# Optimization experiments

Measured on AMD Instinct MI355X. Metric: run time of the kernel, lower is better.

The kernel has to match this reference:

```python
import jax, jax.numpy as jnp
import numpy as np

TEMPERATURE = 0.07
EPS = 1e-12  # matches torch F.normalize eps default

def setup_inputs() -> dict:
    key = jax.random.key(0)
    k1, k2 = jax.random.split(key)
    emb_i = jax.random.normal(k1, (4096, 256), dtype=jnp.float32)
    emb_j = jax.random.normal(k2, (4096, 256), dtype=jnp.float32)
    return {"emb_i": emb_i, "emb_j": emb_j}

def reference(emb_i, emb_j):
    N = emb_i.shape[0]
    # L2-normalize each embedding (F.normalize, dim=1)
    def l2n(x):
        return x / jnp.maximum(jnp.linalg.norm(x, axis=1, keepdims=True), EPS)
    z = jnp.concatenate([l2n(emb_i), l2n(emb_j)], axis=0)  # [2N, D]
    # cosine similarity of normalized rows == plain dot product
    sim = z @ z.T  # [2N, 2N]
    idx = jnp.arange(N)
    pos = jnp.concatenate([sim[idx, idx + N], sim[idx + N, idx]], axis=0)  # [2N]
    exp_sim = jnp.exp(sim / TEMPERATURE)
    # denominator: all entries in the row except the self (diagonal) term
    denom = jnp.sum(exp_sim, axis=1) - jnp.diagonal(exp_sim)  # [2N]
    loss_pair = -(pos / TEMPERATURE) + jnp.log(denom)
    return jnp.sum(loss_pair) / (2 * N)
```

## Files before the change

kernel.cpp:

```cpp
#include <hip/hip_runtime.h>
#include <hip/hip_bf16.h>

#define N_ROWS 4096
#define TWO_N  8192
#define D      256
#define DB     512

#define K_SQRT_SCALE 4.5398159980773926f
#define K_LN2        0.6931471805599453f

#define WAVES        4
#define ROWS_PER_WAVE 64
#define BLOCK_ROWS   (WAVES * ROWS_PER_WAVE)
#define COL_CHUNK    512
#define STAGE_COLS   64
#define NSTAGES      (COL_CHUNK / STAGE_COLS)

typedef __attribute__((ext_vector_type(8))) short short8;
typedef __attribute__((ext_vector_type(4))) float f32x4;

static __device__ inline unsigned short f2bf(float x) {
    __hip_bfloat16 h = __float2bfloat16(x);
    return __builtin_bit_cast(unsigned short, h);
}

__global__ __launch_bounds__(256) void normalize_kernel(
        const float* __restrict__ emb_i, const float* __restrict__ emb_j,
        unsigned short* __restrict__ z, float* __restrict__ S) {
    const int gtid = blockIdx.x * 256 + threadIdx.x;
    if (gtid < TWO_N) S[gtid] = 0.0f;

    const int row  = gtid >> 6;
    const int lane = threadIdx.x & 63;
    if (row >= TWO_N) return;

    const float* src = (row < N_ROWS) ? emb_i + (size_t)row * D
                                      : emb_j + (size_t)(row - N_ROWS) * D;
    float4 v = reinterpret_cast<const float4*>(src)[lane];
    float ss = v.x * v.x + v.y * v.y + v.z * v.z + v.w * v.w;
    #pragma unroll
    for (int m = 1; m < 64; m <<= 1) ss += __shfl_xor(ss, m);
    const float rn = K_SQRT_SCALE / fmaxf(sqrtf(ss), 1e-12f);

    ushort4 o;
    o.x = f2bf(v.x * rn);
    o.y = f2bf(v.y * rn);
    o.z = f2bf(v.z * rn);
    o.w = f2bf(v.w * rn);
    reinterpret_cast<ushort4*>(z + (size_t)row * D)[lane] = o;
}

__global__ __launch_bounds__(256, 2) void simexp_kernel(
        const unsigned short* __restrict__ z,
        float* __restrict__ S, float* __restrict__ posv) {
    __shared__ unsigned short lds[2][STAGE_COLS * D];

    const int tid  = threadIdx.x;
    const int lane = tid & 63;
    const int wave = tid >> 6;
    const int lmod = lane & 15;
    const int lhi  = lane >> 4;

    const int R      = blockIdx.x * BLOCK_ROWS + wave * ROWS_PER_WAVE;
    const int cchunk = blockIdx.y * COL_CHUNK;

    short8 a[4][8];
    #pragma unroll
    for (int s = 0; s < 4; ++s) {
        const unsigned short* arow = z + (size_t)(R + s * 16 + lmod) * D + lhi * 8;
        #pragma unroll
        for (int ks = 0; ks < 8; ++ks)
            a[s][ks] = *reinterpret_cast<const short8*>(arow + ks * 32);
    }

    const int colq = tid >> 5;
    const int offb = (tid & 31) << 4;
    const int soffbase = colq * 512 + (offb ^ (colq << 4));
    const int ldsbase  = tid * 16;

    const char* zbytes = (const char*)z;

    auto stage = [&](int st, int buf) {
        const char* src = zbytes + (size_t)(cchunk + st * STAGE_COLS) * DB + soffbase;
        char* dst = (char*)&lds[buf][0] + ldsbase;
        #pragma unroll
        for (int i = 0; i < 8; ++i) {
            __builtin_amdgcn_global_load_lds(
                (const __attribute__((address_space(1))) unsigned int*)(src + i * 4096),
                (__attribute__((address_space(3))) unsigned int*)(dst + i * 4096),
                16, 0, 0);
        }
    };

    float sums[4][4];
    #pragma unroll
    for (int s = 0; s < 4; ++s)
        #pragma unroll
        for (int r = 0; r < 4; ++r) sums[s][r] = 0.0f;

    stage(0, 0);
    __syncthreads();

    for (int st = 0; st < NSTAGES; ++st) {
        if (st + 1 < NSTAGES) stage(st + 1, (st + 1) & 1);

        const char* base = (const char*)&lds[st & 1][0];
        const int c0 = cchunk + st * STAGE_COLS;

        #pragma unroll
        for (int cs = 0; cs < 4; ++cs) {
            const int colL = cs * 16 + lmod;
            const int swz  = (colL & 7) << 4;
            const char* brow = base + colL * 512;

            f32x4 acc0 = {0.f, 0.f, 0.f, 0.f};
            f32x4 acc1 = {0.f, 0.f, 0.f, 0.f};
            f32x4 acc2 = {0.f, 0.f, 0.f, 0.f};
            f32x4 acc3 = {0.f, 0.f, 0.f, 0.f};
            #pragma unroll
            for (int ks = 0; ks < 8; ++ks) {
                short8 bk = *reinterpret_cast<const short8*>(
                    brow + (((ks * 64 + lhi * 16) ^ swz)));
                acc0 = __builtin_amdgcn_mfma_f32_16x16x32_bf16(a[0][ks], bk, acc0, 0, 0, 0);
                acc1 = __builtin_amdgcn_mfma_f32_16x16x32_bf16(a[1][ks], bk, acc1, 0, 0, 0);
                acc2 = __builtin_amdgcn_mfma_f32_16x16x32_bf16(a[2][ks], bk, acc2, 0, 0, 0);
                acc3 = __builtin_amdgcn_mfma_f32_16x16x32_bf16(a[3][ks], bk, acc3, 0, 0, 0);
            }

            const int csub = c0 + cs * 16;
            f32x4 accs[4] = {acc0, acc1, acc2, acc3};
            #pragma unroll
            for (int s = 0; s < 4; ++s) {
                const int rowt = R + s * 16;
                if (csub == rowt) {
                    #pragma unroll
                    for (int r = 0; r < 4; ++r) {
                        float e = __builtin_amdgcn_exp2f(accs[s][r]);
                        sums[s][r] += (lmod != lhi * 4 + r) ? e : 0.0f;
                    }
                } else if (csub == (rowt ^ N_ROWS)) {
                    #pragma unroll
                    for (int r = 0; r < 4; ++r) {
                        if (lmod == lhi * 4 + r)
                            posv[rowt + lhi * 4 + r] = accs[s][r];
                        sums[s][r] += __builtin_amdgcn_exp2f(accs[s][r]);
                    }
                } else {
                    #pragma unroll
                    for (int r = 0; r < 4; ++r)
                        sums[s][r] += __builtin_amdgcn_exp2f(accs[s][r]);
                }
            }
        }
        __syncthreads();
    }

    #pragma unroll
    for (int s = 0; s < 4; ++s)
        #pragma unroll
        for (int r = 0; r < 4; ++r) {
            float v = sums[s][r];
            v += __shfl_xor(v, 1);
            v += __shfl_xor(v, 2);
            v += __shfl_xor(v, 4);
            v += __shfl_xor(v, 8);
            if (lmod == 0) atomicAdd(&S[R + s * 16 + lhi * 4 + r], v);
        }
}

__global__ __launch_bounds__(1024) void finalize_kernel(
        const float* __restrict__ S, const float* __restrict__ posv,
        float* __restrict__ out) {
    const int tid = threadIdx.x;
    float local = 0.0f;
    #pragma unroll
    for (int i = tid; i < TWO_N; i += 1024)
        local += logf(S[i]) - posv[i] * K_LN2;
    #pragma unroll
    for (int m = 1; m < 64; m <<= 1) local += __shfl_xor(local, m);
    __shared__ float red[16];
    if ((tid & 63) == 0) red[tid >> 6] = local;
    __syncthreads();
    if (tid == 0) {
        float t = 0.0f;
        #pragma unroll
        for (int w = 0; w < 16; ++w) t += red[w];
        out[0] = t / (float)TWO_N;
    }
}

extern "C" void kernel_launch(void* const* d_in, const int* in_sizes, int n_in,
                              void* d_out, int out_size, void* d_ws, size_t ws_size,
                              hipStream_t stream) {
    const float* emb_i = (const float*)d_in[0];
    const float* emb_j = (const float*)d_in[1];
    float* out = (float*)d_out;

    unsigned short* z = (unsigned short*)d_ws;
    float* S    = (float*)((char*)d_ws + (size_t)TWO_N * D * 2);
    float* posv = S + TWO_N;

    normalize_kernel<<<TWO_N / 4, 256, 0, stream>>>(emb_i, emb_j, z, S);
    simexp_kernel<<<dim3(TWO_N / BLOCK_ROWS, TWO_N / COL_CHUNK), 256, 0, stream>>>(z, S, posv);
    finalize_kernel<<<1, 1024, 0, stream>>>(S, posv, out);
}
```

Measured before the change: 48.91 us.

## Restructure sim-exp GEMM into K-sliced tiles with smaller blocks and XCD-aware mapping

```diff
diff --git a/kernel.cpp b/kernel.cpp
--- a/kernel.cpp
+++ b/kernel.cpp
@@ -9,12 +9,14 @@
 #define K_SQRT_SCALE 4.5398159980773926f
 #define K_LN2        0.6931471805599453f
 
-#define WAVES        4
 #define ROWS_PER_WAVE 64
-#define BLOCK_ROWS   (WAVES * ROWS_PER_WAVE)
-#define COL_CHUNK    512
-#define STAGE_COLS   64
-#define NSTAGES      (COL_CHUNK / STAGE_COLS)
+#define BLOCK_ROWS    256
+#define COLS_PER_BLK  64
+#define KSLICE        32
+#define NKT           8
+#define ROW_TILES     (TWO_N / BLOCK_ROWS)
+#define COL_TILES     (TWO_N / COLS_PER_BLK)
+#define NBLOCKS       (ROW_TILES * COL_TILES)
 
 typedef __attribute__((ext_vector_type(8))) short short8;
 typedef __attribute__((ext_vector_type(4))) float f32x4;
@@ -50,10 +52,10 @@
     reinterpret_cast<ushort4*>(z + (size_t)row * D)[lane] = o;
 }
 
-__global__ __launch_bounds__(256, 2) void simexp_kernel(
+__global__ __launch_bounds__(256, 4) void simexp_kernel(
         const unsigned short* __restrict__ z,
         float* __restrict__ S, float* __restrict__ posv) {
-    __shared__ unsigned short lds[2][STAGE_COLS * D];
+    __shared__ unsigned short lds[2][COLS_PER_BLK * KSLICE];
 
     const int tid  = threadIdx.x;
     const int lane = tid & 63;
@@ -61,36 +63,72 @@
     const int lmod = lane & 15;
     const int lhi  = lane >> 4;
 
-    const int R      = blockIdx.x * BLOCK_ROWS + wave * ROWS_PER_WAVE;
-    const int cchunk = blockIdx.y * COL_CHUNK;
-
-    short8 a[4][8];
-    #pragma unroll
-    for (int s = 0; s < 4; ++s) {
-        const unsigned short* arow = z + (size_t)(R + s * 16 + lmod) * D + lhi * 8;
-        #pragma unroll
-        for (int ks = 0; ks < 8; ++ks)
-            a[s][ks] = *reinterpret_cast<const short8*>(arow + ks * 32);
+    const int wgid    = (blockIdx.x & 7) * (NBLOCKS / 8) + (blockIdx.x >> 3);
+    const int rowtile = wgid >> 7;
+    const int coltile = wgid & (COL_TILES - 1);
+    const int R = rowtile * BLOCK_ROWS + wave * ROWS_PER_WAVE;
+    const int C = coltile * COLS_PER_BLK;
+
+    const char* zb = (const char*)z;
+
+    const size_t ssrc = (size_t)(C + (tid >> 2)) * DB + (size_t)((tid & 3) * 16);
+    const int    sdst = tid * 16;
+
+    f32x4 acc[4][4];
+    #pragma unroll
+    for (int s = 0; s < 4; ++s)
+        #pragma unroll
+        for (int c = 0; c < 4; ++c) acc[s][c] = (f32x4){0.f, 0.f, 0.f, 0.f};
+
+    short8 aA[4], aB[4];
+
+#define STAGE_B(kt, buf)                                                        \
+    __builtin_amdgcn_global_load_lds(                                           \
+        (const __attribute__((address_space(1))) unsigned int*)(zb + ssrc + (kt) * 64), \
+        (__attribute__((address_space(3))) unsigned int*)((char*)&lds[buf][0] + sdst),  \
+        16, 0, 0)
+
+#define LOAD_A(kt, dst)                                                         \
+    _Pragma("unroll")                                                           \
+    for (int s = 0; s < 4; ++s)                                                 \
+        dst[s] = *reinterpret_cast<const short8*>(                              \
+            zb + (size_t)(R + s * 16 + lmod) * DB + (kt) * 64 + lhi * 16)
+
+#define COMPUTE(buf, a)                                                         \
+    do {                                                                        \
+        const char* base_ = (const char*)&lds[buf][0] + lhi * 16;               \
+        __builtin_amdgcn_s_setprio(1);                                          \
+        _Pragma("unroll")                                                       \
+        for (int cs = 0; cs < 4; ++cs) {                                        \
+            short8 b_ = *reinterpret_cast<const short8*>(base_ + (cs * 16 + lmod) * 64); \
+            _Pragma("unroll")                                                   \
+            for (int s = 0; s < 4; ++s)                                         \
+                acc[s][cs] = __builtin_amdgcn_mfma_f32_16x16x32_bf16(a[s], b_, acc[s][cs], 0, 0, 0); \
+        }                                                                       \
+        __builtin_amdgcn_s_setprio(0);                                          \
+    } while (0)
+
+    STAGE_B(0, 0);
+    LOAD_A(0, aA);
+    __syncthreads();
+
+    for (int t = 0; t < 4; ++t) {
+        STAGE_B(2 * t + 1, 1);
+        LOAD_A(2 * t + 1, aB);
+        COMPUTE(0, aA);
+        __syncthreads();
+
+        if (t < 3) {
+            STAGE_B(2 * t + 2, 0);
+            LOAD_A(2 * t + 2, aA);
+        }
+        COMPUTE(1, aB);
+        __syncthreads();
     }
 
-    const int colq = tid >> 5;
-    const int offb = (tid & 31) << 4;
-    const int soffbase = colq * 512 + (offb ^ (colq << 4));
-    const int ldsbase  = tid * 16;
-
-    const char* zbytes = (const char*)z;
-
-    auto stage = [&](int st, int buf) {
-        const char* src = zbytes + (size_t)(cchunk + st * STAGE_COLS) * DB + soffbase;
-        char* dst = (char*)&lds[buf][0] + ldsbase;
-        #pragma unroll
-        for (int i = 0; i < 8; ++i) {
-            __builtin_amdgcn_global_load_lds(
-                (const __attribute__((address_space(1))) unsigned int*)(src + i * 4096),
-                (__attribute__((address_space(3))) unsigned int*)(dst + i * 4096),
-                16, 0, 0);
-        }
-    };
+#undef STAGE_B
+#undef LOAD_A
+#undef COMPUTE
 
     float sums[4][4];
     #pragma unroll
@@ -98,61 +136,31 @@
         #pragma unroll
         for (int r = 0; r < 4; ++r) sums[s][r] = 0.0f;
 
-    stage(0, 0);
-    __syncthreads();
-
-    for (int st = 0; st < NSTAGES; ++st) {
-        if (st + 1 < NSTAGES) stage(st + 1, (st + 1) & 1);
-
-        const char* base = (const char*)&lds[st & 1][0];
-        const int c0 = cchunk + st * STAGE_COLS;
-
-        #pragma unroll
-        for (int cs = 0; cs < 4; ++cs) {
-            const int colL = cs * 16 + lmod;
-            const int swz  = (colL & 7) << 4;
-            const char* brow = base + colL * 512;
-
-            f32x4 acc0 = {0.f, 0.f, 0.f, 0.f};
-            f32x4 acc1 = {0.f, 0.f, 0.f, 0.f};
-            f32x4 acc2 = {0.f, 0.f, 0.f, 0.f};
-            f32x4 acc3 = {0.f, 0.f, 0.f, 0.f};
-            #pragma unroll
-            for (int ks = 0; ks < 8; ++ks) {
-                short8 bk = *reinterpret_cast<const short8*>(
-                    brow + (((ks * 64 + lhi * 16) ^ swz)));
-                acc0 = __builtin_amdgcn_mfma_f32_16x16x32_bf16(a[0][ks], bk, acc0, 0, 0, 0);
-                acc1 = __builtin_amdgcn_mfma_f32_16x16x32_bf16(a[1][ks], bk, acc1, 0, 0, 0);
-                acc2 = __builtin_amdgcn_mfma_f32_16x16x32_bf16(a[2][ks], bk, acc2, 0, 0, 0);
-                acc3 = __builtin_amdgcn_mfma_f32_16x16x32_bf16(a[3][ks], bk, acc3, 0, 0, 0);
-            }
-
-            const int csub = c0 + cs * 16;
-            f32x4 accs[4] = {acc0, acc1, acc2, acc3};
-            #pragma unroll
-            for (int s = 0; s < 4; ++s) {
-                const int rowt = R + s * 16;
-                if (csub == rowt) {
-                    #pragma unroll
-                    for (int r = 0; r < 4; ++r) {
-                        float e = __builtin_amdgcn_exp2f(accs[s][r]);
-                        sums[s][r] += (lmod != lhi * 4 + r) ? e : 0.0f;
-                    }
-                } else if (csub == (rowt ^ N_ROWS)) {
-                    #pragma unroll
-                    for (int r = 0; r < 4; ++r) {
-                        if (lmod == lhi * 4 + r)
-                            posv[rowt + lhi * 4 + r] = accs[s][r];
-                        sums[s][r] += __builtin_amdgcn_exp2f(accs[s][r]);
-                    }
-                } else {
-                    #pragma unroll
-                    for (int r = 0; r < 4; ++r)
-                        sums[s][r] += __builtin_amdgcn_exp2f(accs[s][r]);
+    #pragma unroll
+    for (int cs = 0; cs < 4; ++cs) {
+        const int csub = C + cs * 16;
+        #pragma unroll
+        for (int s = 0; s < 4; ++s) {
+            const int rowt = R + s * 16;
+            if (csub == rowt) {
+                #pragma unroll
+                for (int r = 0; r < 4; ++r) {
+                    float e = __builtin_amdgcn_exp2f(acc[s][cs][r]);
+                    sums[s][r] += (lmod != lhi * 4 + r) ? e : 0.0f;
                 }
+            } else if (csub == (rowt ^ N_ROWS)) {
+                #pragma unroll
+                for (int r = 0; r < 4; ++r) {
+                    if (lmod == lhi * 4 + r)
+                        posv[rowt + lhi * 4 + r] = acc[s][cs][r];
+                    sums[s][r] += __builtin_amdgcn_exp2f(acc[s][cs][r]);
+                }
+            } else {
+                #pragma unroll
+                for (int r = 0; r < 4; ++r)
+                    sums[s][r] += __builtin_amdgcn_exp2f(acc[s][cs][r]);
             }
         }
-        __syncthreads();
     }
 
     #pragma unroll
@@ -201,6 +209,6 @@
     float* posv = S + TWO_N;
 
     normalize_kernel<<<TWO_N / 4, 256, 0, stream>>>(emb_i, emb_j, z, S);
-    simexp_kernel<<<dim3(TWO_N / BLOCK_ROWS, TWO_N / COL_CHUNK), 256, 0, stream>>>(z, S, posv);
+    simexp_kernel<<<NBLOCKS, 256, 0, stream>>>(z, S, posv);
     finalize_kernel<<<1, 1024, 0, stream>>>(S, posv, out);
 }
```

New measurement: 92.01 us. 1.88x slower.
